# Kernel optimization log

Hardware: AMD Instinct MI355X
Metric: run time of the kernel (lower is better)

The kernel has to match this reference:

```python
import jax, jax.numpy as jnp
from jax import lax
import numpy as np

B, C, H, W, HID = 16, 8, 512, 512, 16


def setup_inputs() -> dict:
    key = jax.random.key(0)
    k1, k2, k3, k4, k5 = jax.random.split(key, 5)
    x = jax.random.normal(k1, (B, C, H, W), dtype=jnp.float32)
    w1_w = jax.random.normal(k2, (HID, 4 * C), dtype=jnp.float32) * 0.1  # 1x1 conv 32->16
    w1_b = jax.random.normal(k3, (HID,), dtype=jnp.float32) * 0.1
    w2_w = jax.random.normal(k4, (C, HID), dtype=jnp.float32) * 0.1     # 1x1 conv 16->8, no bias
    update_mask = jax.random.randint(k5, (B, 1, H, W), 0, 2, dtype=jnp.int32)  # floor(rand+0.5)
    return {"x": x, "w1_w": w1_w, "w1_b": w1_b, "w2_w": w2_w, "update_mask": update_mask}


def _fixed_filters(dtype):
    ident = jnp.zeros((3, 3), dtype).at[1, 1].set(1.0)
    sobel_x = jnp.array([[-1.0, 0.0, 1.0], [-2.0, 0.0, 2.0], [-1.0, 0.0, 1.0]], dtype) / 8.0
    lap = jnp.array([[1.0, 2.0, 1.0], [2.0, -12.0, 2.0], [1.0, 2.0, 1.0]], dtype) / 16.0
    return jnp.stack([ident, sobel_x, sobel_x.T, lap])  # [4,3,3]


def _perception(x):
    b, c, h, w = x.shape
    filt = _fixed_filters(x.dtype)
    xp = jnp.pad(x, ((0, 0), (0, 0), (1, 1), (1, 1)), mode="wrap")  # circular pad
    y = lax.conv_general_dilated(
        xp.reshape(b * c, 1, h + 2, w + 2), filt[:, None], (1, 1), "VALID",
        dimension_numbers=("NCHW", "OIHW", "NCHW"))  # [b*c,4,h,w]
    return y.reshape(b, c * 4, h, w)  # channel-major: (c0f0..c0f3, c1f0.., ...)


def reference(x, w1_w, w1_b, w2_w, update_mask):
    dt = 1.0
    y = _perception(x)                                   # [B,4C,H,W]
    y = jax.nn.relu(jnp.einsum("bchw,oc->bohw", y, w1_w) + w1_b[None, :, None, None])
    y = jnp.einsum("bchw,oc->bohw", y, w2_w)             # [B,C,H,W]
    return x + dt * y * update_mask.astype(x.dtype)
```

## Files before the change

kernel.cpp:

```cpp
#include <hip/hip_runtime.h>
#include <stdint.h>


constexpr int B = 16, C = 8, H = 512, W = 512, HID = 16;
constexpr int HW = H * W;

constexpr int ROWF = 520;
constexpr int CHF  = 4 * ROWF + 8;
constexpr int XTOT = 8 * CHF;
constexpr int MOFF = XTOT;
constexpr int LDSF = XTOT + 2 * 512;

typedef __attribute__((ext_vector_type(8))) short bf16x8;
typedef __attribute__((ext_vector_type(4))) float f32x4;
typedef const __attribute__((address_space(1))) void* as1cp;
typedef __attribute__((address_space(3))) void* as3p;

__device__ __host__ inline uint32_t bf16rne(float f) {
    const uint32_t u = __float_as_uint(f);
    return (u + 0x7fffu + ((u >> 16) & 1u)) >> 16;
}
__device__ inline float bf16tof(uint32_t hs) { return __uint_as_float(hs << 16); }

__device__ inline uint32_t pkbf(float a, float b) {
    const uint32_t ua = __float_as_uint(a);
    const uint32_t ub = __float_as_uint(b);
    const uint32_t ra = ua + 0x7fffu + ((ua >> 16) & 1u);
    const uint32_t rb = ub + 0x7fffu + ((ub >> 16) & 1u);
    return __builtin_amdgcn_perm(rb, ra, 0x07060302u);
}

__global__ void repack(const float* __restrict__ w1w,
                       const float* __restrict__ w1b,
                       const float* __restrict__ w2w,
                       float* __restrict__ wdf) {
    uint32_t* wd = (uint32_t*)wdf;
    const int t = threadIdx.x;
    if (t >= 64) return;
    const int h = t & 15, kg = t >> 4;
    uint32_t whi[4] = {0, 0, 0, 0}, wlo[4] = {0, 0, 0, 0}, w2f[4] = {0, 0, 0, 0};
    for (int j = 0; j < 8; ++j) {
        const int k = kg * 8 + j, ch = k >> 2, f = k & 3;
        const float* wr = w1w + h * 32 + ch * 4;
        const float we = (f == 0) ? (wr[0] - wr[3])
                       : (f == 3) ? wr[3] * 0.0625f
                                  : wr[f] * 0.125f;
        const uint32_t hs = bf16rne(we);
        const uint32_t ls = bf16rne(we - bf16tof(hs));
        whi[j >> 1] |= hs << (16 * (j & 1));
        wlo[j >> 1] |= ls << (16 * (j & 1));
    }
    for (int j = 0; j < 4; ++j) {
        const float v = (h < 8) ? w2w[h * 16 + kg * 4 + j] : 0.0f;
        w2f[j >> 1] |= bf16rne(v) << (16 * (j & 1));
    }
    for (int q = 0; q < 4; ++q) {
        wd[t * 4 + q]       = whi[q];
        wd[256 + t * 4 + q] = wlo[q];
        wd[512 + t * 4 + q] = w2f[q];
    }
    if (t < 16) wdf[768 + t] = w1b[t];
}

__global__ __launch_bounds__(512, 4) void nca_step_kernel(
    const float* __restrict__ x,
    const int*   __restrict__ mask,
    float*       __restrict__ out,
    const float* __restrict__ wdf)
{
    __shared__ float S[LDSF];

    const int bid = blockIdx.x;
    const int l   = (bid & 7) * 512 + (bid >> 3);
    const int b   = l >> 8;
    const int y0  = (l & 255) << 1;

    const int tid  = threadIdx.x;
    const int lane = tid & 63;
    const int wv   = tid >> 6;

    const float* xb = x + (size_t)b * C * HW;
    const int*   mb = mask + (size_t)b * HW;

    union { uint4 u; bf16x8 v; } whiU, wloU, w2U;
    whiU.u = ((const uint4*)wdf)[lane];
    wloU.u = ((const uint4*)wdf)[64 + lane];
    w2U.u  = ((const uint4*)wdf)[128 + lane];
    const f32x4 bias4 = ((const f32x4*)(wdf + 768))[lane >> 4];

    for (int c = wv; c < 68; c += 8) {
        if (c < 64) {
            const int r = c >> 1, hf = c & 1;
            const int ch = r >> 2, rs = r & 3;
            const int grow = (y0 - 1 + rs) & (H - 1);
            const float* src = xb + ch * HW + grow * W + hf * 256 + lane * 4;
            float* dst = S + ch * CHF + rs * ROWF + 4 + hf * 256;
            __builtin_amdgcn_global_load_lds((as1cp)src, (as3p)dst, 16, 0, 0);
        } else {
            const int mr = (c - 64) >> 1, hf = c & 1;
            const int* src = mb + (y0 + mr) * W + hf * 256 + lane * 4;
            float* dst = S + MOFF + mr * 512 + hf * 256;
            __builtin_amdgcn_global_load_lds((as1cp)src, (as3p)dst, 16, 0, 0);
        }
    }
    __syncthreads();
    if (tid < 64) {
        const int r = tid >> 1;
        float* rb = S + (r >> 2) * CHF + (r & 3) * ROWF;
        if (tid & 1) rb[516] = rb[4];
        else         rb[3]   = rb[515];
    }
    __syncthreads();

    const int rel = wv >> 2;
    const int y   = y0 + rel;
    const int grp = lane >> 4;
    const int p   = lane & 15;
    const int chA = grp * 2;
    float* ob = out + (size_t)b * C * HW;

#pragma unroll 2
    for (int i = 0; i < 8; ++i) {
        const int g  = (wv & 3) + i * 4;
        const int px = g * 16 + p;
        const int ci = px + 3;

        float f_[8];
#pragma unroll
        for (int cc = 0; cc < 2; ++cc) {
            const float* R0 = S + (chA + cc) * CHF + rel * ROWF + ci;
            const float* R1 = R0 + ROWF;
            const float* R2 = R1 + ROWF;
            const float a0 = R0[0], a1 = R0[1], a2 = R0[2];
            const float b0 = R1[0], b1 = R1[1], b2 = R1[2];
            const float c0 = R2[0], c1 = R2[1], c2 = R2[2];
            const float s0 = fmaf(2.f, b0, a0 + c0);
            const float s1 = fmaf(2.f, b1, a1 + c1);
            const float s2 = fmaf(2.f, b2, a2 + c2);
            const float d0 = c0 - a0, d1 = c1 - a1, d2 = c2 - a2;
            f_[cc * 4 + 0] = b1;
            f_[cc * 4 + 1] = s2 - s0;
            f_[cc * 4 + 2] = fmaf(2.f, d1, d0 + d2);
            f_[cc * 4 + 3] = fmaf(2.f, s1, s0 + s2);
        }

        union { uint32_t u[4]; bf16x8 v; } bh = {{
            pkbf(f_[0], f_[1]), pkbf(f_[2], f_[3]),
            pkbf(f_[4], f_[5]), pkbf(f_[6], f_[7])}};

        f32x4 acc = bias4;
        acc = __builtin_amdgcn_mfma_f32_16x16x32_bf16(whiU.v, bh.v, acc, 0, 0, 0);
        acc = __builtin_amdgcn_mfma_f32_16x16x32_bf16(wloU.v, bh.v, acc, 0, 0, 0);

        union { uint32_t u[4]; bf16x8 v; } b2 = {{
            pkbf(fmaxf(acc[0], 0.f), fmaxf(acc[1], 0.f)),
            pkbf(fmaxf(acc[2], 0.f), fmaxf(acc[3], 0.f)), 0, 0}};
        f32x4 d2 = {0.f, 0.f, 0.f, 0.f};
        d2 = __builtin_amdgcn_mfma_f32_16x16x32_bf16(w2U.v, b2.v, d2, 0, 0, 0);

        if (lane < 32) {
            const float mfv =
                (float)((const int*)(S + MOFF))[rel * 512 + px];
            const int och0 = grp * 4;
            float* op = ob + y * W + px;
#pragma unroll
            for (int r = 0; r < 4; ++r) {
                const float xv =
                    S[(och0 + r) * CHF + (rel + 1) * ROWF + 4 + px];
                op[(och0 + r) * HW] = fmaf(d2[r], mfv, xv);
            }
        }
    }
}

extern "C" void kernel_launch(void* const* d_in, const int* in_sizes, int n_in,
                              void* d_out, int out_size, void* d_ws, size_t ws_size,
                              hipStream_t stream) {
    const float* x    = (const float*)d_in[0];
    const float* w1w  = (const float*)d_in[1];
    const float* w1b  = (const float*)d_in[2];
    const float* w2w  = (const float*)d_in[3];
    const int*   mask = (const int*)d_in[4];
    float* out = (float*)d_out;
    float* wdf = (float*)d_ws;

    hipLaunchKernelGGL(repack, dim3(1), dim3(64), 0, stream,
                       w1w, w1b, w2w, wdf);
    hipLaunchKernelGGL(nca_step_kernel, dim3(B * H / 2), dim3(512), 0, stream,
                       x, mask, out, wdf);
}
```

Baseline: 80.67 us.

## Load mask directly to registers, simplify LDS fill, use hardware bf16 pack

The update mask is no longer staged through LDS. Each lane loads its eight mask values straight from global memory into registers before the x tile load. The x tile load is restructured so each wave issues eight unrolled LDS-direct loads with no branch. The manual round-to-nearest bf16 packing is replaced with the HIP intrinsic, which can map to a hardware packed-convert instruction on gfx950, and the main loop is fully unrolled. This shrinks LDS usage and instruction count, at the cost of more live registers and less coalesced mask loads (16-element strided segments).

Measured after the change: 83.60 us. 1.04x slower.

```diff
diff --git a/kernel.cpp b/kernel.cpp
--- a/kernel.cpp
+++ b/kernel.cpp
@@ -1,4 +1,5 @@
 #include <hip/hip_runtime.h>
+#include <hip/hip_bf16.h>
 #include <stdint.h>
 
 
@@ -7,9 +8,7 @@
 
 constexpr int ROWF = 520;
 constexpr int CHF  = 4 * ROWF + 8;
-constexpr int XTOT = 8 * CHF;
-constexpr int MOFF = XTOT;
-constexpr int LDSF = XTOT + 2 * 512;
+constexpr int LDSF = 8 * CHF;
 
 typedef __attribute__((ext_vector_type(8))) short bf16x8;
 typedef __attribute__((ext_vector_type(4))) float f32x4;
@@ -22,12 +21,10 @@
 }
 __device__ inline float bf16tof(uint32_t hs) { return __uint_as_float(hs << 16); }
 
-__device__ inline uint32_t pkbf(float a, float b) {
-    const uint32_t ua = __float_as_uint(a);
-    const uint32_t ub = __float_as_uint(b);
-    const uint32_t ra = ua + 0x7fffu + ((ua >> 16) & 1u);
-    const uint32_t rb = ub + 0x7fffu + ((ub >> 16) & 1u);
-    return __builtin_amdgcn_perm(rb, ra, 0x07060302u);
+__device__ inline uint32_t pk2(float a, float b) {
+    union { __hip_bfloat162 h; uint32_t u; } r;
+    r.h = __float22bfloat162_rn(make_float2(a, b));
+    return r.u;
 }
 
 __global__ void repack(const float* __restrict__ w1w,
@@ -82,24 +79,33 @@
     const float* xb = x + (size_t)b * C * HW;
     const int*   mb = mask + (size_t)b * HW;
 
+    const int rel = wv >> 2;
+    const int y   = y0 + rel;
+    const int grp = lane >> 4;
+    const int p   = lane & 15;
+    const int chA = grp * 2;
+
+    int msk[8];
+#pragma unroll
+    for (int i = 0; i < 8; ++i)
+        msk[i] = mb[y * W + ((wv & 3) + 4 * i) * 16 + p];
+
     union { uint4 u; bf16x8 v; } whiU, wloU, w2U;
     whiU.u = ((const uint4*)wdf)[lane];
     wloU.u = ((const uint4*)wdf)[64 + lane];
     w2U.u  = ((const uint4*)wdf)[128 + lane];
     const f32x4 bias4 = ((const f32x4*)(wdf + 768))[lane >> 4];
 
-    for (int c = wv; c < 68; c += 8) {
-        if (c < 64) {
-            const int r = c >> 1, hf = c & 1;
-            const int ch = r >> 2, rs = r & 3;
-            const int grow = (y0 - 1 + rs) & (H - 1);
-            const float* src = xb + ch * HW + grow * W + hf * 256 + lane * 4;
-            float* dst = S + ch * CHF + rs * ROWF + 4 + hf * 256;
-            __builtin_amdgcn_global_load_lds((as1cp)src, (as3p)dst, 16, 0, 0);
-        } else {
-            const int mr = (c - 64) >> 1, hf = c & 1;
-            const int* src = mb + (y0 + mr) * W + hf * 256 + lane * 4;
-            float* dst = S + MOFF + mr * 512 + hf * 256;
+    {
+        const int rs   = (wv >> 1) & 3;
+        const int hf   = wv & 1;
+        const int grow = (y0 - 1 + rs) & (H - 1);
+        const int goff = grow * W + hf * 256 + lane * 4;
+        const int loff = rs * ROWF + 4 + hf * 256;
+#pragma unroll
+        for (int ch = 0; ch < 8; ++ch) {
+            const float* src = xb + ch * HW + goff;
+            float* dst = S + ch * CHF + loff;
             __builtin_amdgcn_global_load_lds((as1cp)src, (as3p)dst, 16, 0, 0);
         }
     }
@@ -112,14 +118,9 @@
     }
     __syncthreads();
 
-    const int rel = wv >> 2;
-    const int y   = y0 + rel;
-    const int grp = lane >> 4;
-    const int p   = lane & 15;
-    const int chA = grp * 2;
     float* ob = out + (size_t)b * C * HW;
 
-#pragma unroll 2
+#pragma unroll
     for (int i = 0; i < 8; ++i) {
         const int g  = (wv & 3) + i * 4;
         const int px = g * 16 + p;
@@ -145,22 +146,21 @@
         }
 
         union { uint32_t u[4]; bf16x8 v; } bh = {{
-            pkbf(f_[0], f_[1]), pkbf(f_[2], f_[3]),
-            pkbf(f_[4], f_[5]), pkbf(f_[6], f_[7])}};
+            pk2(f_[0], f_[1]), pk2(f_[2], f_[3]),
+            pk2(f_[4], f_[5]), pk2(f_[6], f_[7])}};
 
         f32x4 acc = bias4;
         acc = __builtin_amdgcn_mfma_f32_16x16x32_bf16(whiU.v, bh.v, acc, 0, 0, 0);
         acc = __builtin_amdgcn_mfma_f32_16x16x32_bf16(wloU.v, bh.v, acc, 0, 0, 0);
 
         union { uint32_t u[4]; bf16x8 v; } b2 = {{
-            pkbf(fmaxf(acc[0], 0.f), fmaxf(acc[1], 0.f)),
-            pkbf(fmaxf(acc[2], 0.f), fmaxf(acc[3], 0.f)), 0, 0}};
+            pk2(fmaxf(acc[0], 0.f), fmaxf(acc[1], 0.f)),
+            pk2(fmaxf(acc[2], 0.f), fmaxf(acc[3], 0.f)), 0, 0}};
         f32x4 d2 = {0.f, 0.f, 0.f, 0.f};
         d2 = __builtin_amdgcn_mfma_f32_16x16x32_bf16(w2U.v, b2.v, d2, 0, 0, 0);
 
         if (lane < 32) {
-            const float mfv =
-                (float)((const int*)(S + MOFF))[rel * 512 + px];
+            const float mfv = (float)msk[i];
             const int och0 = grp * 4;
             float* op = ob + y * W + px;
 #pragma unroll
```

## Split row staging into two halves and overlap second-half loads with compute

Applied to the files above, without the earlier changes.

Staging of each block's input rows is split into two column halves. The first half and the wrap and halo columns are loaded, then a barrier, and the left-half pixels are computed while the right half's async global-to-LDS loads are still in flight. A second barrier precedes the right-half compute. The halo columns are read directly from global memory instead of being copied inside LDS, which removes one barrier from the prologue. The aim is to hide the load latency inside each block, though with four blocks per CU there may already be enough overlap across blocks.

New measurement: 84.49 us. 4.7% more time.

```diff
diff --git a/kernel.cpp b/kernel.cpp
--- a/kernel.cpp
+++ b/kernel.cpp
@@ -82,35 +82,46 @@
     const float* xb = x + (size_t)b * C * HW;
     const int*   mb = mask + (size_t)b * HW;
 
+    const int rs   = wv & 3;
+    const int chW  = wv >> 2;
+    const int grow = (y0 - 1 + rs) & (H - 1);
+
+#define STAGE_HALF(hf) do {                                                \
+    const int goff = grow * W + (hf) * 256 + lane * 4;                     \
+    const int loff = rs * ROWF + 4 + (hf) * 256;                           \
+    _Pragma("unroll") for (int cq = 0; cq < 4; ++cq) {                     \
+        const int ch = chW + cq * 2;                                       \
+        __builtin_amdgcn_global_load_lds((as1cp)(xb + ch * HW + goff),     \
+                                         (as3p)(S + ch * CHF + loff),      \
+                                         16, 0, 0);                        \
+    }                                                                      \
+    if (wv < 2) {                          \
+        const int* msrc = mb + (y0 + wv) * W + (hf) * 256 + lane * 4;      \
+        float* mdst = S + MOFF + wv * 512 + (hf) * 256;                    \
+        __builtin_amdgcn_global_load_lds((as1cp)msrc, (as3p)mdst,          \
+                                         16, 0, 0);                        \
+    } } while (0)
+
+    STAGE_HALF(0);
+    if (tid < 96) {
+        const int set = tid >> 5;
+        const int r   = tid & 31;
+        const int hch = r >> 2, hrs = r & 3;
+        const int hrow = (y0 - 1 + hrs) & (H - 1);
+        const int col  = (set == 0) ? 511 : ((set == 1) ? 0 : 256);
+        const int slot = (set == 0) ? 3 : ((set == 1) ? 516 : 260);
+        S[hch * CHF + hrs * ROWF + slot] = xb[hch * HW + hrow * W + col];
+    }
+    __syncthreads();
+
+    STAGE_HALF(1);
+#undef STAGE_HALF
+
     union { uint4 u; bf16x8 v; } whiU, wloU, w2U;
     whiU.u = ((const uint4*)wdf)[lane];
     wloU.u = ((const uint4*)wdf)[64 + lane];
     w2U.u  = ((const uint4*)wdf)[128 + lane];
     const f32x4 bias4 = ((const f32x4*)(wdf + 768))[lane >> 4];
-
-    for (int c = wv; c < 68; c += 8) {
-        if (c < 64) {
-            const int r = c >> 1, hf = c & 1;
-            const int ch = r >> 2, rs = r & 3;
-            const int grow = (y0 - 1 + rs) & (H - 1);
-            const float* src = xb + ch * HW + grow * W + hf * 256 + lane * 4;
-            float* dst = S + ch * CHF + rs * ROWF + 4 + hf * 256;
-            __builtin_amdgcn_global_load_lds((as1cp)src, (as3p)dst, 16, 0, 0);
-        } else {
-            const int mr = (c - 64) >> 1, hf = c & 1;
-            const int* src = mb + (y0 + mr) * W + hf * 256 + lane * 4;
-            float* dst = S + MOFF + mr * 512 + hf * 256;
-            __builtin_amdgcn_global_load_lds((as1cp)src, (as3p)dst, 16, 0, 0);
-        }
-    }
-    __syncthreads();
-    if (tid < 64) {
-        const int r = tid >> 1;
-        float* rb = S + (r >> 2) * CHF + (r & 3) * ROWF;
-        if (tid & 1) rb[516] = rb[4];
-        else         rb[3]   = rb[515];
-    }
-    __syncthreads();
 
     const int rel = wv >> 2;
     const int y   = y0 + rel;
@@ -119,58 +130,53 @@
     const int chA = grp * 2;
     float* ob = out + (size_t)b * C * HW;
 
+#define BODY(i) do {                                                       \
+    const int g  = (wv & 3) + (i) * 4;                                     \
+    const int px = g * 16 + p;                                             \
+    const int ci = px + 3;                        \
+    float f_[8];                                                           \
+    _Pragma("unroll") for (int cc = 0; cc < 2; ++cc) {                     \
+        const float* R0 = S + (chA + cc) * CHF + rel * ROWF + ci;          \
+        const float* R1 = R0 + ROWF;                                       \
+        const float* R2 = R1 + ROWF;                                       \
+        const float a0 = R0[0], a1 = R0[1], a2 = R0[2];                    \
+        const float b0 = R1[0], b1 = R1[1], b2 = R1[2];                    \
+        const float c0 = R2[0], c1 = R2[1], c2 = R2[2];                    \
+        const float s0 = fmaf(2.f, b0, a0 + c0);                           \
+        const float s1 = fmaf(2.f, b1, a1 + c1);                           \
+        const float s2 = fmaf(2.f, b2, a2 + c2);                           \
+        const float d0 = c0 - a0, d1 = c1 - a1, d2 = c2 - a2;              \
+        f_[cc * 4 + 0] = b1;                                               \
+        f_[cc * 4 + 1] = s2 - s0;                                          \
+        f_[cc * 4 + 2] = fmaf(2.f, d1, d0 + d2);                           \
+        f_[cc * 4 + 3] = fmaf(2.f, s1, s0 + s2); }                         \
+    union { uint32_t u[4]; bf16x8 v; } bh = {{                             \
+        pkbf(f_[0], f_[1]), pkbf(f_[2], f_[3]),                            \
+        pkbf(f_[4], f_[5]), pkbf(f_[6], f_[7])}};                          \
+    f32x4 acc = bias4;                                                     \
+    acc = __builtin_amdgcn_mfma_f32_16x16x32_bf16(whiU.v, bh.v, acc, 0, 0, 0); \
+    acc = __builtin_amdgcn_mfma_f32_16x16x32_bf16(wloU.v, bh.v, acc, 0, 0, 0); \
+    union { uint32_t u[4]; bf16x8 v; } b2 = {{                             \
+        pkbf(fmaxf(acc[0], 0.f), fmaxf(acc[1], 0.f)),                      \
+        pkbf(fmaxf(acc[2], 0.f), fmaxf(acc[3], 0.f)), 0, 0}};              \
+    f32x4 d2 = {0.f, 0.f, 0.f, 0.f};                                       \
+    d2 = __builtin_amdgcn_mfma_f32_16x16x32_bf16(w2U.v, b2.v, d2, 0, 0, 0); \
+    if (lane < 32) {                                                       \
+        const float mfv = (float)((const int*)(S + MOFF))[rel * 512 + px]; \
+        const int och0 = grp * 4;                                          \
+        float* op = ob + y * W + px;                                       \
+        _Pragma("unroll") for (int r = 0; r < 4; ++r) {                    \
+            const float xv = S[(och0 + r) * CHF + (rel + 1) * ROWF + 4 + px]; \
+            op[(och0 + r) * HW] = fmaf(d2[r], mfv, xv); } } } while (0)
+
 #pragma unroll 2
-    for (int i = 0; i < 8; ++i) {
-        const int g  = (wv & 3) + i * 4;
-        const int px = g * 16 + p;
-        const int ci = px + 3;
+    for (int i = 0; i < 4; ++i) BODY(i);
 
-        float f_[8];
-#pragma unroll
-        for (int cc = 0; cc < 2; ++cc) {
-            const float* R0 = S + (chA + cc) * CHF + rel * ROWF + ci;
-            const float* R1 = R0 + ROWF;
-            const float* R2 = R1 + ROWF;
-            const float a0 = R0[0], a1 = R0[1], a2 = R0[2];
-            const float b0 = R1[0], b1 = R1[1], b2 = R1[2];
-            const float c0 = R2[0], c1 = R2[1], c2 = R2[2];
-            const float s0 = fmaf(2.f, b0, a0 + c0);
-            const float s1 = fmaf(2.f, b1, a1 + c1);
-            const float s2 = fmaf(2.f, b2, a2 + c2);
-            const float d0 = c0 - a0, d1 = c1 - a1, d2 = c2 - a2;
-            f_[cc * 4 + 0] = b1;
-            f_[cc * 4 + 1] = s2 - s0;
-            f_[cc * 4 + 2] = fmaf(2.f, d1, d0 + d2);
-            f_[cc * 4 + 3] = fmaf(2.f, s1, s0 + s2);
-        }
+    __syncthreads();
 
-        union { uint32_t u[4]; bf16x8 v; } bh = {{
-            pkbf(f_[0], f_[1]), pkbf(f_[2], f_[3]),
-            pkbf(f_[4], f_[5]), pkbf(f_[6], f_[7])}};
-
-        f32x4 acc = bias4;
-        acc = __builtin_amdgcn_mfma_f32_16x16x32_bf16(whiU.v, bh.v, acc, 0, 0, 0);
-        acc = __builtin_amdgcn_mfma_f32_16x16x32_bf16(wloU.v, bh.v, acc, 0, 0, 0);
-
-        union { uint32_t u[4]; bf16x8 v; } b2 = {{
-            pkbf(fmaxf(acc[0], 0.f), fmaxf(acc[1], 0.f)),
-            pkbf(fmaxf(acc[2], 0.f), fmaxf(acc[3], 0.f)), 0, 0}};
-        f32x4 d2 = {0.f, 0.f, 0.f, 0.f};
-        d2 = __builtin_amdgcn_mfma_f32_16x16x32_bf16(w2U.v, b2.v, d2, 0, 0, 0);
-
-        if (lane < 32) {
-            const float mfv =
-                (float)((const int*)(S + MOFF))[rel * 512 + px];
-            const int och0 = grp * 4;
-            float* op = ob + y * W + px;
-#pragma unroll
-            for (int r = 0; r < 4; ++r) {
-                const float xv =
-                    S[(och0 + r) * CHF + (rel + 1) * ROWF + 4 + px];
-                op[(och0 + r) * HW] = fmaf(d2[r], mfv, xv);
-            }
-        }
-    }
+#pragma unroll 2
+    for (int i = 4; i < 8; ++i) BODY(i);
+#undef BODY
 }
 
 extern "C" void kernel_launch(void* const* d_in, const int* in_sizes, int n_in,
```
